# Optimization experiments

Hardware: AMD Instinct MI355X
Metric: run time of the kernel (lower is better)

Reference implementation:

```python
import jax, jax.numpy as jnp
import numpy as np

EPS = 1e-5

def conv1d(x, w, stride=2):
    # x: [N, Cin, L], w: [Cout, Cin, K], VALID padding
    return jax.lax.conv_general_dilated(x, w, (stride,), 'VALID',
                                         dimension_numbers=('NCH', 'OIH', 'NCH'))

def ln(x, g, b):
    # LayerNorm over last dim
    mu = jnp.mean(x, axis=-1, keepdims=True)
    var = jnp.mean((x - mu) ** 2, axis=-1, keepdims=True)
    return (x - mu) * jax.lax.rsqrt(var + EPS) * g + b

def block(x, w, g, b):
    return jax.nn.relu(ln(conv1d(x, w), g, b))

def setup_inputs() -> dict:
    key = jax.random.key(0)
    ks = jax.random.split(key, 20)
    B, CH, H, W = 4096, 143, 8, 8
    def p(k, shape, fan_in):
        return jax.random.normal(k, shape, dtype=jnp.float32) * (1.0 / np.sqrt(fan_in))
    inp = {
        'x': jax.random.normal(ks[0], (B, CH, H, W), dtype=jnp.float32),
        'w1': p(ks[1], (16, 2, 3), 6),
        'w2': p(ks[2], (28, 16, 3), 48),
        'w3': p(ks[3], (28, 28, 3), 84),
        'w4': p(ks[4], (28, 28, 3), 84),
        'f1': p(ks[5], (4, 2, 3), 6),
        'f2': p(ks[6], (4, 4, 3), 12),
        'f3': p(ks[7], (4, 4, 3), 12),
        'f4': p(ks[8], (4, 4, 3), 12),
        'ln1_w': jnp.ones((71,), jnp.float32), 'ln1_b': jnp.zeros((71,), jnp.float32),
        'ln2_w': jnp.ones((35,), jnp.float32), 'ln2_b': jnp.zeros((35,), jnp.float32),
        'ln3_w': jnp.ones((17,), jnp.float32), 'ln3_b': jnp.zeros((17,), jnp.float32),
        'ln4_w': jnp.ones((8,), jnp.float32), 'ln4_b': jnp.zeros((8,), jnp.float32),
    }
    return inp

def reference(x, w1, w2, w3, w4, f1, f2, f3, f4,
              ln1_w, ln1_b, ln2_w, ln2_b, ln3_w, ln3_b, ln4_w, ln4_b):
    b, ch, h, w = x.shape
    cr = x[:, :, 3:5, :]   # [b, ch, 2, w]
    cc = x[:, :, :, 3:5]   # [b, ch, h, 2]
    # FFT magnitude along spectral axis (axis=1)
    cr_fft = jnp.abs(jnp.fft.fft(cr, axis=1)).astype(jnp.float32)
    cc_fft = jnp.abs(jnp.fft.fft(cc, axis=1)).astype(jnp.float32)
    # reshape to [b*w (or b*h), 2, ch] sequences
    cr = jnp.transpose(cr, (0, 2, 3, 1)).reshape(b * w, 2, ch)
    cc = jnp.transpose(cc, (0, 2, 3, 1)).reshape(b * h, 2, ch)
    cr_fft = jnp.transpose(cr_fft, (0, 2, 3, 1)).reshape(b * w, 2, ch)
    cc_fft = jnp.transpose(cc_fft, (0, 2, 3, 1)).reshape(b * h, 2, ch)
    # spatial towers: 143 -> 71 -> 35 -> 17 -> 8, channels 2->16->28->28->28
    cr = block(cr, w1, ln1_w, ln1_b); cc = block(cc, w1, ln1_w, ln1_b)
    cr = block(cr, w2, ln2_w, ln2_b); cc = block(cc, w2, ln2_w, ln2_b)
    cr = block(cr, w3, ln3_w, ln3_b); cc = block(cc, w3, ln3_w, ln3_b)
    cr = block(cr, w4, ln4_w, ln4_b); cc = block(cc, w4, ln4_w, ln4_b)
    # fft towers: channels 2->4->4->4->4
    cr_fft = block(cr_fft, f1, ln1_w, ln1_b); cc_fft = block(cc_fft, f1, ln1_w, ln1_b)
    cr_fft = block(cr_fft, f2, ln2_w, ln2_b); cc_fft = block(cc_fft, f2, ln2_w, ln2_b)
    cr_fft = block(cr_fft, f3, ln3_w, ln3_b); cc_fft = block(cc_fft, f3, ln3_w, ln3_b)
    cr_fft = block(cr_fft, f4, ln4_w, ln4_b); cc_fft = block(cc_fft, f4, ln4_w, ln4_b)
    cr = jnp.transpose(cr.reshape(b, w, -1, 8), (0, 2, 1, 3))          # [b,28,w,8]
    cc = jnp.transpose(cc.reshape(b, h, -1, 8), (0, 2, 1, 3))          # [b,28,h,8]
    cr_fft = jnp.transpose(cr_fft.reshape(b, w, -1, 8), (0, 2, 1, 3))  # [b,4,w,8]
    cc_fft = jnp.transpose(cc_fft.reshape(b, h, -1, 8), (0, 2, 1, 3))  # [b,4,h,8]
    return jnp.concatenate([cr, cc, cr_fft, cc_fft], axis=1)           # [b,64,8,8]
```

## Files before the change

kernel.cpp:

```cpp
#include <hip/hip_runtime.h>
#include <math.h>

typedef _Float16 h16;
typedef _Float16 h16x2 __attribute__((ext_vector_type(2)));

#define NS 65536
#define VSTR 131072

__global__ __launch_bounds__(256) void k_gather(const float* __restrict__ x,
                                                float* __restrict__ xv,
                                                float* __restrict__ tw) {
  const int b = blockIdx.x;
  if (b < 4096) {
    const float* xb = x + (size_t)b * 9152;
    const int base = b * 32;
    for (int i = threadIdx.x; i < 9152; i += 256) {
      float v = xb[i];
      int c = i >> 6, pos = i & 63;
      if (pos >= 24 && pos < 40)
        xv[(size_t)c * VSTR + base + (pos - 24)] = v;
      int wc = pos & 7;
      if (wc == 3 || wc == 4)
        xv[(size_t)c * VSTR + base + 16 + ((pos >> 3) << 1) + (wc - 3)] = v;
    }
  } else {
    for (int i = threadIdx.x; i < 10296; i += 256) {
      int k = i / 143, n = i - k * 143;
      int e = (k * n) % 143;
      float ang = 6.2831853071795864769f * (float)e / 143.0f;
      float s, c;
      sincosf(ang, &s, &c);
      tw[2 * i] = c;
      tw[2 * i + 1] = s;
    }
  }
}

__global__ __launch_bounds__(256, 2) void k_dft(const float* __restrict__ xv,
                                                const float* __restrict__ tw,
                                                h16* __restrict__ fm) {
  const int v = blockIdx.x * 256 + threadIdx.x;
  float xr[143];
#pragma unroll
  for (int n = 0; n < 143; ++n) xr[n] = xv[(size_t)n * VSTR + v];

  for (int k = 0; k < 72; ++k) {
    const float* __restrict__ twk = tw + k * 286;
    float re = 0.f, im = 0.f;
#pragma unroll
    for (int n = 0; n < 143; ++n) {
      re = fmaf(xr[n], twk[2 * n], re);
      im = fmaf(xr[n], twk[2 * n + 1], im);
    }
    float m = sqrtf(re * re + im * im);
    fm[(size_t)k * VSTR + v] = (h16)m;
    if (k) fm[(size_t)(143 - k) * VSTR + v] = (h16)m;
  }
}

__device__ __forceinline__ void smap(int& d, int& w, int& va, int& vb,
                                     int& bi, int& u) {
  int lane = threadIdx.x & 63;
  w = __builtin_amdgcn_readfirstlane(threadIdx.x >> 6);
  d = (int)blockIdx.x * 64 + lane;
  bi = d >> 4;
  u = d & 15;
  va = (u < 8) ? bi * 32 + ((u >> 2) << 3) + ((u & 3) << 1)
               : bi * 32 + 16 + ((u & 7) << 1);
  vb = va + 1;
}

__global__ __launch_bounds__(256, 2) void k_c1(const float* __restrict__ xv,
                                               const h16* __restrict__ fm,
                                               const float* __restrict__ w1,
                                               const float* __restrict__ f1,
                                               float* __restrict__ s1) {
  int d, w, va, vb, bi, u;
  smap(d, w, va, vb, bi, u);

  {
    float sum[4] = {0, 0, 0, 0}, sq[4] = {0, 0, 0, 0};
    float A0 = xv[va], B0 = xv[vb];
    for (int p = 0; p < 71; ++p) {
      float A1 = xv[(size_t)(2 * p + 1) * VSTR + va];
      float A2 = xv[(size_t)(2 * p + 2) * VSTR + va];
      float B1 = xv[(size_t)(2 * p + 1) * VSTR + vb];
      float B2 = xv[(size_t)(2 * p + 2) * VSTR + vb];
#pragma unroll
      for (int j = 0; j < 4; ++j) {
        const float* wp = w1 + (4 * w + j) * 6;
        float v = A0 * wp[0];
        v = fmaf(A1, wp[1], v); v = fmaf(A2, wp[2], v);
        v = fmaf(B0, wp[3], v); v = fmaf(B1, wp[4], v); v = fmaf(B2, wp[5], v);
        sum[j] += v; sq[j] = fmaf(v, v, sq[j]);
      }
      A0 = A2; B0 = B2;
    }
#pragma unroll
    for (int j = 0; j < 4; ++j) {
      float mu = sum[j] * (1.0f / 71.0f);
      float var = sq[j] * (1.0f / 71.0f) - mu * mu;
      s1[(size_t)(4 * w + j) * NS + d] = mu;
      s1[(size_t)(16 + 4 * w + j) * NS + d] = rsqrtf(var + 1e-5f);
    }
  }
  {
    float sum = 0.f, sq = 0.f;
    const float* wp = f1 + w * 6;
    float A0 = (float)fm[va], B0 = (float)fm[vb];
    for (int p = 0; p < 71; ++p) {
      float A1 = (float)fm[(size_t)(2 * p + 1) * VSTR + va];
      float A2 = (float)fm[(size_t)(2 * p + 2) * VSTR + va];
      float B1 = (float)fm[(size_t)(2 * p + 1) * VSTR + vb];
      float B2 = (float)fm[(size_t)(2 * p + 2) * VSTR + vb];
      float v = A0 * wp[0];
      v = fmaf(A1, wp[1], v); v = fmaf(A2, wp[2], v);
      v = fmaf(B0, wp[3], v); v = fmaf(B1, wp[4], v); v = fmaf(B2, wp[5], v);
      sum += v; sq = fmaf(v, v, sq);
      A0 = A2; B0 = B2;
    }
    float mu = sum * (1.0f / 71.0f);
    float var = sq * (1.0f / 71.0f) - mu * mu;
    s1[(size_t)(32 + w) * NS + d] = mu;
    s1[(size_t)(36 + w) * NS + d] = rsqrtf(var + 1e-5f);
  }
}

__global__ __launch_bounds__(256, 2) void k_c2(const float* __restrict__ xv,
                                               const h16* __restrict__ fm,
                                               const float* __restrict__ w1,
                                               const float* __restrict__ w2,
                                               const float* __restrict__ f1,
                                               const float* __restrict__ f2,
                                               const float* __restrict__ l1g,
                                               const float* __restrict__ l1b,
                                               const float* __restrict__ s1,
                                               h16* __restrict__ z2,
                                               float* __restrict__ s2) {
  __shared__ float red[4][32][64];
  const int lane = threadIdx.x & 63;
  const int w = threadIdx.x >> 6;
  const int d = (int)blockIdx.x * 64 + lane;
  const int bi = d >> 4, u = d & 15;
  const int va = (u < 8) ? bi * 32 + ((u >> 2) << 3) + ((u & 3) << 1)
                         : bi * 32 + 16 + ((u & 7) << 1);
  const int ps = w * 9;
  const int pe = (ps + 9 < 35) ? (ps + 9) : 35;

  float sum[28], sq[28];
  float sums[4], sqs[4];

  {
    float mu1[16], inv1[16];
#pragma unroll
    for (int c = 0; c < 16; ++c) {
      mu1[c] = s1[(size_t)c * NS + d];
      inv1[c] = s1[(size_t)(16 + c) * NS + d];
    }
#pragma unroll
    for (int j = 0; j < 28; ++j) { sum[j] = 0.f; sq[j] = 0.f; }

    float n0[16], n1[16], n2[16];
    float a2, b2, a3, b3, a4, b4, a5, b5, a6, b6;

    {
      float2 r0 = *(const float2*)(xv + (size_t)(4 * ps) * VSTR + va);
      float2 r1 = *(const float2*)(xv + (size_t)(4 * ps + 1) * VSTR + va);
      float2 r2 = *(const float2*)(xv + (size_t)(4 * ps + 2) * VSTR + va);
      a2 = r2.x; b2 = r2.y;
      const float gg = l1g[2 * ps], bb = l1b[2 * ps];
#pragma unroll
      for (int c = 0; c < 16; ++c) {
        const float* wp = w1 + c * 6;
        float v = r0.x * wp[0];
        v = fmaf(r1.x, wp[1], v); v = fmaf(a2, wp[2], v);
        v = fmaf(r0.y, wp[3], v); v = fmaf(r1.y, wp[4], v); v = fmaf(b2, wp[5], v);
        n0[c] = fmaxf(fmaf((v - mu1[c]) * inv1[c], gg, bb), 0.f);
      }
      float2 r3 = *(const float2*)(xv + (size_t)(4 * ps + 3) * VSTR + va);
      float2 r4 = *(const float2*)(xv + (size_t)(4 * ps + 4) * VSTR + va);
      float2 r5 = *(const float2*)(xv + (size_t)(4 * ps + 5) * VSTR + va);
      float2 r6 = *(const float2*)(xv + (size_t)(4 * ps + 6) * VSTR + va);
      a3 = r3.x; b3 = r3.y; a4 = r4.x; b4 = r4.y;
      a5 = r5.x; b5 = r5.y; a6 = r6.x; b6 = r6.y;
    }

#pragma unroll 1
    for (int p = ps; p < pe; ++p) {
      {
        const float gg = l1g[2 * p + 1], bb = l1b[2 * p + 1];
#pragma unroll
        for (int c = 0; c < 16; ++c) {
          const float* wp = w1 + c * 6;
          float v = a2 * wp[0];
          v = fmaf(a3, wp[1], v); v = fmaf(a4, wp[2], v);
          v = fmaf(b2, wp[3], v); v = fmaf(b3, wp[4], v); v = fmaf(b4, wp[5], v);
          n1[c] = fmaxf(fmaf((v - mu1[c]) * inv1[c], gg, bb), 0.f);
        }
      }
      {
        const float gg = l1g[2 * p + 2], bb = l1b[2 * p + 2];
#pragma unroll
        for (int c = 0; c < 16; ++c) {
          const float* wp = w1 + c * 6;
          float v = a4 * wp[0];
          v = fmaf(a5, wp[1], v); v = fmaf(a6, wp[2], v);
          v = fmaf(b4, wp[3], v); v = fmaf(b5, wp[4], v); v = fmaf(b6, wp[5], v);
          n2[c] = fmaxf(fmaf((v - mu1[c]) * inv1[c], gg, bb), 0.f);
        }
      }
      a2 = a6; b2 = b6;
      {
        const int rbase = (p < 34) ? (4 * p + 7) : 139;
        const float* rp = xv + (size_t)rbase * VSTR + va;
        float2 r3 = *(const float2*)(rp);
        float2 r4 = *(const float2*)(rp + (size_t)VSTR);
        float2 r5 = *(const float2*)(rp + (size_t)2 * VSTR);
        float2 r6 = *(const float2*)(rp + (size_t)3 * VSTR);
        a3 = r3.x; b3 = r3.y; a4 = r4.x; b4 = r4.y;
        a5 = r5.x; b5 = r5.y; a6 = r6.x; b6 = r6.y;
      }
#pragma unroll
      for (int j = 0; j < 28; ++j) {
        const float* wp = w2 + j * 48;
        float acc = 0.f;
#pragma unroll
        for (int ci = 0; ci < 16; ++ci) {
          acc = fmaf(n0[ci], wp[ci * 3 + 0], acc);
          acc = fmaf(n1[ci], wp[ci * 3 + 1], acc);
          acc = fmaf(n2[ci], wp[ci * 3 + 2], acc);
        }
        z2[(size_t)(j * 35 + p) * NS + d] = (h16)acc;
        sum[j] += acc; sq[j] = fmaf(acc, acc, sq[j]);
      }
#pragma unroll
      for (int c = 0; c < 16; ++c) n0[c] = n2[c];
    }
  }

  {
    float mu1[4], inv1[4];
#pragma unroll
    for (int c = 0; c < 4; ++c) {
      mu1[c] = s1[(size_t)(32 + c) * NS + d];
      inv1[c] = s1[(size_t)(36 + c) * NS + d];
    }
#pragma unroll
    for (int c = 0; c < 4; ++c) { sums[c] = 0.f; sqs[c] = 0.f; }
    float n0[4], n1[4], n2[4];
    float a2, b2, a3, b3, a4, b4, a5, b5, a6, b6;

    {
      h16x2 r0 = *(const h16x2*)(fm + (size_t)(4 * ps) * VSTR + va);
      h16x2 r1 = *(const h16x2*)(fm + (size_t)(4 * ps + 1) * VSTR + va);
      h16x2 r2 = *(const h16x2*)(fm + (size_t)(4 * ps + 2) * VSTR + va);
      float a0 = (float)r0.x, b0 = (float)r0.y;
      float a1 = (float)r1.x, b1 = (float)r1.y;
      a2 = (float)r2.x; b2 = (float)r2.y;
      const float gg = l1g[2 * ps], bb = l1b[2 * ps];
#pragma unroll
      for (int c = 0; c < 4; ++c) {
        const float* wp = f1 + c * 6;
        float v = a0 * wp[0];
        v = fmaf(a1, wp[1], v); v = fmaf(a2, wp[2], v);
        v = fmaf(b0, wp[3], v); v = fmaf(b1, wp[4], v); v = fmaf(b2, wp[5], v);
        n0[c] = fmaxf(fmaf((v - mu1[c]) * inv1[c], gg, bb), 0.f);
      }
      h16x2 r3 = *(const h16x2*)(fm + (size_t)(4 * ps + 3) * VSTR + va);
      h16x2 r4 = *(const h16x2*)(fm + (size_t)(4 * ps + 4) * VSTR + va);
      h16x2 r5 = *(const h16x2*)(fm + (size_t)(4 * ps + 5) * VSTR + va);
      h16x2 r6 = *(const h16x2*)(fm + (size_t)(4 * ps + 6) * VSTR + va);
      a3 = (float)r3.x; b3 = (float)r3.y; a4 = (float)r4.x; b4 = (float)r4.y;
      a5 = (float)r5.x; b5 = (float)r5.y; a6 = (float)r6.x; b6 = (float)r6.y;
    }

#pragma unroll 1
    for (int p = ps; p < pe; ++p) {
      {
        const float gg = l1g[2 * p + 1], bb = l1b[2 * p + 1];
#pragma unroll
        for (int c = 0; c < 4; ++c) {
          const float* wp = f1 + c * 6;
          float v = a2 * wp[0];
          v = fmaf(a3, wp[1], v); v = fmaf(a4, wp[2], v);
          v = fmaf(b2, wp[3], v); v = fmaf(b3, wp[4], v); v = fmaf(b4, wp[5], v);
          n1[c] = fmaxf(fmaf((v - mu1[c]) * inv1[c], gg, bb), 0.f);
        }
      }
      {
        const float gg = l1g[2 * p + 2], bb = l1b[2 * p + 2];
#pragma unroll
        for (int c = 0; c < 4; ++c) {
          const float* wp = f1 + c * 6;
          float v = a4 * wp[0];
          v = fmaf(a5, wp[1], v); v = fmaf(a6, wp[2], v);
          v = fmaf(b4, wp[3], v); v = fmaf(b5, wp[4], v); v = fmaf(b6, wp[5], v);
          n2[c] = fmaxf(fmaf((v - mu1[c]) * inv1[c], gg, bb), 0.f);
        }
      }
      a2 = a6; b2 = b6;
      {
        const int rbase = (p < 34) ? (4 * p + 7) : 139;
        const h16* rp = fm + (size_t)rbase * VSTR + va;
        h16x2 r3 = *(const h16x2*)(rp);
        h16x2 r4 = *(const h16x2*)(rp + (size_t)VSTR);
        h16x2 r5 = *(const h16x2*)(rp + (size_t)2 * VSTR);
        h16x2 r6 = *(const h16x2*)(rp + (size_t)3 * VSTR);
        a3 = (float)r3.x; b3 = (float)r3.y; a4 = (float)r4.x; b4 = (float)r4.y;
        a5 = (float)r5.x; b5 = (float)r5.y; a6 = (float)r6.x; b6 = (float)r6.y;
      }
#pragma unroll
      for (int co = 0; co < 4; ++co) {
        const float* wpo = f2 + co * 12;
        float acc = 0.f;
#pragma unroll
        for (int c = 0; c < 4; ++c) acc = fmaf(n0[c], wpo[c * 3 + 0], acc);
#pragma unroll
        for (int c = 0; c < 4; ++c) acc = fmaf(n1[c], wpo[c * 3 + 1], acc);
#pragma unroll
        for (int c = 0; c < 4; ++c) acc = fmaf(n2[c], wpo[c * 3 + 2], acc);
        z2[(size_t)(980 + co * 35 + p) * NS + d] = (h16)acc;
        sums[co] += acc; sqs[co] = fmaf(acc, acc, sqs[co]);
      }
#pragma unroll
      for (int c = 0; c < 4; ++c) n0[c] = n2[c];
    }
  }

#pragma unroll
  for (int j = 0; j < 28; ++j) red[w][j][lane] = sum[j];
#pragma unroll
  for (int c = 0; c < 4; ++c) red[w][28 + c][lane] = sums[c];
  __syncthreads();
  const int jb = 7 * w;
  float fs[7], fq[7];
#pragma unroll
  for (int t = 0; t < 7; ++t)
    fs[t] = red[0][jb + t][lane] + red[1][jb + t][lane] +
            red[2][jb + t][lane] + red[3][jb + t][lane];
  float fss = red[0][28 + w][lane] + red[1][28 + w][lane] +
              red[2][28 + w][lane] + red[3][28 + w][lane];
  __syncthreads();
#pragma unroll
  for (int j = 0; j < 28; ++j) red[w][j][lane] = sq[j];
#pragma unroll
  for (int c = 0; c < 4; ++c) red[w][28 + c][lane] = sqs[c];
  __syncthreads();
#pragma unroll
  for (int t = 0; t < 7; ++t)
    fq[t] = red[0][jb + t][lane] + red[1][jb + t][lane] +
            red[2][jb + t][lane] + red[3][jb + t][lane];
  float fqs = red[0][28 + w][lane] + red[1][28 + w][lane] +
              red[2][28 + w][lane] + red[3][28 + w][lane];
#pragma unroll
  for (int t = 0; t < 7; ++t) {
    float mu = fs[t] * (1.0f / 35.0f);
    float var = fq[t] * (1.0f / 35.0f) - mu * mu;
    s2[(size_t)(jb + t) * NS + d] = mu;
    s2[(size_t)(28 + jb + t) * NS + d] = rsqrtf(var + 1e-5f);
  }
  {
    float mu = fss * (1.0f / 35.0f);
    float var = fqs * (1.0f / 35.0f) - mu * mu;
    s2[(size_t)(56 + w) * NS + d] = mu;
    s2[(size_t)(60 + w) * NS + d] = rsqrtf(var + 1e-5f);
  }
}

__global__ __launch_bounds__(256, 1) void k_c3(const h16* __restrict__ z2,
                                               const float* __restrict__ w3,
                                               const float* __restrict__ f3,
                                               const float* __restrict__ l2g,
                                               const float* __restrict__ l2b,
                                               const float* __restrict__ s2,
                                               h16* __restrict__ z3,
                                               float* __restrict__ s3) {
  int d, w, va, vb, bi, u;
  smap(d, w, va, vb, bi, u);

  {
    float acc[7][17];
#pragma unroll
    for (int j = 0; j < 7; ++j)
#pragma unroll
      for (int p = 0; p < 17; ++p) acc[j][p] = 0.f;
    const int cobase = 7 * w;
#pragma unroll 1
    for (int ci = 0; ci < 28; ++ci) {
      float mu = s2[(size_t)ci * NS + d];
      float inv = s2[(size_t)(28 + ci) * NS + d];
      float n[35];
#pragma unroll
      for (int t = 0; t < 35; ++t) {
        float raw = (float)z2[(size_t)(ci * 35 + t) * NS + d];
        n[t] = fmaxf(fmaf((raw - mu) * inv, l2g[t], l2b[t]), 0.f);
      }
#pragma unroll
      for (int j = 0; j < 7; ++j) {
        const float* wp = w3 + (cobase + j) * 84 + ci * 3;
        float w0 = wp[0], w1v = wp[1], w2v = wp[2];
#pragma unroll
        for (int p = 0; p < 17; ++p)
          acc[j][p] = fmaf(n[2 * p], w0,
                      fmaf(n[2 * p + 1], w1v,
                      fmaf(n[2 * p + 2], w2v, acc[j][p])));
      }
    }
#pragma unroll
    for (int j = 0; j < 7; ++j) {
      const int co = cobase + j;
      float sum = 0.f, sq = 0.f;
#pragma unroll
      for (int p = 0; p < 17; ++p) {
        sum += acc[j][p]; sq = fmaf(acc[j][p], acc[j][p], sq);
        z3[(size_t)(co * 17 + p) * NS + d] = (h16)acc[j][p];
      }
      float mu = sum * (1.0f / 17.0f);
      float var = sq * (1.0f / 17.0f) - mu * mu;
      s3[(size_t)co * NS + d] = mu;
      s3[(size_t)(28 + co) * NS + d] = rsqrtf(var + 1e-5f);
    }
  }
  {
    float acc[17];
#pragma unroll
    for (int p = 0; p < 17; ++p) acc[p] = 0.f;
    const int co = w;
#pragma unroll 1
    for (int ci = 0; ci < 4; ++ci) {
      float mu = s2[(size_t)(56 + ci) * NS + d];
      float inv = s2[(size_t)(60 + ci) * NS + d];
      float n[35];
#pragma unroll
      for (int t = 0; t < 35; ++t) {
        float raw = (float)z2[(size_t)(980 + ci * 35 + t) * NS + d];
        n[t] = fmaxf(fmaf((raw - mu) * inv, l2g[t], l2b[t]), 0.f);
      }
      const float* wp = f3 + co * 12 + ci * 3;
      float w0 = wp[0], w1v = wp[1], w2v = wp[2];
#pragma unroll
      for (int p = 0; p < 17; ++p)
        acc[p] = fmaf(n[2 * p], w0,
                 fmaf(n[2 * p + 1], w1v,
                 fmaf(n[2 * p + 2], w2v, acc[p])));
    }
    float sum = 0.f, sq = 0.f;
#pragma unroll
    for (int p = 0; p < 17; ++p) {
      sum += acc[p]; sq = fmaf(acc[p], acc[p], sq);
      z3[(size_t)(476 + co * 17 + p) * NS + d] = (h16)acc[p];
    }
    float mu = sum * (1.0f / 17.0f);
    float var = sq * (1.0f / 17.0f) - mu * mu;
    s3[(size_t)(56 + co) * NS + d] = mu;
    s3[(size_t)(60 + co) * NS + d] = rsqrtf(var + 1e-5f);
  }
}

__global__ __launch_bounds__(256, 1) void k_c4(const h16* __restrict__ z3,
                                               const float* __restrict__ w4,
                                               const float* __restrict__ f4,
                                               const float* __restrict__ l3g,
                                               const float* __restrict__ l3b,
                                               const float* __restrict__ l4g,
                                               const float* __restrict__ l4b,
                                               const float* __restrict__ s3,
                                               float* __restrict__ out) {
  int d, w, va, vb, bi, u;
  smap(d, w, va, vb, bi, u);

  {
    float acc[7][8];
#pragma unroll
    for (int j = 0; j < 7; ++j)
#pragma unroll
      for (int p = 0; p < 8; ++p) acc[j][p] = 0.f;
    const int cobase = 7 * w;
#pragma unroll 1
    for (int ci = 0; ci < 28; ++ci) {
      float mu = s3[(size_t)ci * NS + d];
      float inv = s3[(size_t)(28 + ci) * NS + d];
      float n[17];
#pragma unroll
      for (int t = 0; t < 17; ++t) {
        float raw = (float)z3[(size_t)(ci * 17 + t) * NS + d];
        n[t] = fmaxf(fmaf((raw - mu) * inv, l3g[t], l3b[t]), 0.f);
      }
#pragma unroll
      for (int j = 0; j < 7; ++j) {
        const float* wp = w4 + (cobase + j) * 84 + ci * 3;
        float w0 = wp[0], w1v = wp[1], w2v = wp[2];
#pragma unroll
        for (int p = 0; p < 8; ++p)
          acc[j][p] = fmaf(n[2 * p], w0,
                      fmaf(n[2 * p + 1], w1v,
                      fmaf(n[2 * p + 2], w2v, acc[j][p])));
      }
    }
#pragma unroll
    for (int j = 0; j < 7; ++j) {
      const int co = cobase + j;
      float sum = 0.f, sq = 0.f;
#pragma unroll
      for (int p = 0; p < 8; ++p) { sum += acc[j][p]; sq = fmaf(acc[j][p], acc[j][p], sq); }
      float mu = sum * 0.125f;
      float var = sq * 0.125f - mu * mu;
      float inv = rsqrtf(var + 1e-5f);
      const int ch = (u < 8) ? co : (28 + co);
      float* op = out + (size_t)bi * 4096 + (size_t)ch * 64 + (size_t)(u & 7) * 8;
      float o[8];
#pragma unroll
      for (int p = 0; p < 8; ++p)
        o[p] = fmaxf(fmaf((acc[j][p] - mu) * inv, l4g[p], l4b[p]), 0.f);
      *(float4*)(op) = make_float4(o[0], o[1], o[2], o[3]);
      *(float4*)(op + 4) = make_float4(o[4], o[5], o[6], o[7]);
    }
  }
  {
    float acc[8];
#pragma unroll
    for (int p = 0; p < 8; ++p) acc[p] = 0.f;
    const int co = w;
#pragma unroll 1
    for (int ci = 0; ci < 4; ++ci) {
      float mu = s3[(size_t)(56 + ci) * NS + d];
      float inv = s3[(size_t)(60 + ci) * NS + d];
      float n[17];
#pragma unroll
      for (int t = 0; t < 17; ++t) {
        float raw = (float)z3[(size_t)(476 + ci * 17 + t) * NS + d];
        n[t] = fmaxf(fmaf((raw - mu) * inv, l3g[t], l3b[t]), 0.f);
      }
      const float* wp = f4 + co * 12 + ci * 3;
      float w0 = wp[0], w1v = wp[1], w2v = wp[2];
#pragma unroll
      for (int p = 0; p < 8; ++p)
        acc[p] = fmaf(n[2 * p], w0,
                 fmaf(n[2 * p + 1], w1v,
                 fmaf(n[2 * p + 2], w2v, acc[p])));
    }
    float sum = 0.f, sq = 0.f;
#pragma unroll
    for (int p = 0; p < 8; ++p) { sum += acc[p]; sq = fmaf(acc[p], acc[p], sq); }
    float mu = sum * 0.125f;
    float var = sq * 0.125f - mu * mu;
    float inv = rsqrtf(var + 1e-5f);
    const int ch = (u < 8) ? (56 + co) : (60 + co);
    float* op = out + (size_t)bi * 4096 + (size_t)ch * 64 + (size_t)(u & 7) * 8;
    float o[8];
#pragma unroll
    for (int p = 0; p < 8; ++p)
      o[p] = fmaxf(fmaf((acc[p] - mu) * inv, l4g[p], l4b[p]), 0.f);
    *(float4*)(op) = make_float4(o[0], o[1], o[2], o[3]);
    *(float4*)(op + 4) = make_float4(o[4], o[5], o[6], o[7]);
  }
}

extern "C" void kernel_launch(void* const* d_in, const int* in_sizes, int n_in,
                              void* d_out, int out_size, void* d_ws, size_t ws_size,
                              hipStream_t stream) {
  const float* x   = (const float*)d_in[0];
  const float* w1  = (const float*)d_in[1];
  const float* w2  = (const float*)d_in[2];
  const float* w3  = (const float*)d_in[3];
  const float* w4  = (const float*)d_in[4];
  const float* f1  = (const float*)d_in[5];
  const float* f2  = (const float*)d_in[6];
  const float* f3  = (const float*)d_in[7];
  const float* f4  = (const float*)d_in[8];
  const float* l1g = (const float*)d_in[9];
  const float* l1b = (const float*)d_in[10];
  const float* l2g = (const float*)d_in[11];
  const float* l2b = (const float*)d_in[12];
  const float* l3g = (const float*)d_in[13];
  const float* l3b = (const float*)d_in[14];
  const float* l4g = (const float*)d_in[15];
  const float* l4b = (const float*)d_in[16];
  float* out = (float*)d_out;
  char* wsb = (char*)d_ws;

  float* xv = (float*)(wsb + 0);
  h16*   fm = (h16*)(wsb + 74973184ull);
  h16*   z2 = (h16*)(wsb + 112459776ull);
  h16*   z3 = (h16*)(wsb + 259260416ull);
  float* s1 = (float*)(wsb + 330563584ull);
  float* s2 = (float*)(wsb + 341049344ull);
  float* s3 = (float*)(wsb + 357826560ull);
  float* tw = (float*)(wsb + 374603776ull);

  k_gather<<<4097, 256, 0, stream>>>(x, xv, tw);
  k_dft<<<512, 256, 0, stream>>>(xv, tw, fm);
  k_c1<<<1024, 256, 0, stream>>>(xv, fm, w1, f1, s1);
  k_c2<<<1024, 256, 0, stream>>>(xv, fm, w1, w2, f1, f2, l1g, l1b, s1, z2, s2);
  k_c3<<<1024, 256, 0, stream>>>(z2, w3, f3, l2g, l2b, s2, z3, s3);
  k_c4<<<1024, 256, 0, stream>>>(z3, w4, f4, l3g, l3b, l4g, l4b, s3, out);
}
```

Before: 1.161 ms.

## Fuse conv3 and conv4 stages into one kernel via shared-memory staging

Merges the third and fourth conv+LayerNorm stages into a single kernel. Normalized layer-3 activations are staged in LDS as fp16 instead of writing z3 and its statistics to global memory and reading them back. This removes a kernel launch and a large global round trip. In exchange the kernel takes more LDS, adds block barriers, and raises launch bounds to two blocks per CU, which may pressure registers given the large accumulator arrays.

```diff
diff --git a/kernel.cpp b/kernel.cpp
--- a/kernel.cpp
+++ b/kernel.cpp
@@ -367,16 +367,25 @@
   }
 }
 
-__global__ __launch_bounds__(256, 1) void k_c3(const h16* __restrict__ z2,
-                                               const float* __restrict__ w3,
-                                               const float* __restrict__ f3,
-                                               const float* __restrict__ l2g,
-                                               const float* __restrict__ l2b,
-                                               const float* __restrict__ s2,
-                                               h16* __restrict__ z3,
-                                               float* __restrict__ s3) {
-  int d, w, va, vb, bi, u;
-  smap(d, w, va, vb, bi, u);
+__global__ __launch_bounds__(256, 2) void k_c34(const h16* __restrict__ z2,
+                                                const float* __restrict__ w3,
+                                                const float* __restrict__ w4,
+                                                const float* __restrict__ f3,
+                                                const float* __restrict__ f4,
+                                                const float* __restrict__ l2g,
+                                                const float* __restrict__ l2b,
+                                                const float* __restrict__ l3g,
+                                                const float* __restrict__ l3b,
+                                                const float* __restrict__ l4g,
+                                                const float* __restrict__ l4b,
+                                                const float* __restrict__ s2,
+                                                float* __restrict__ out) {
+  __shared__ h16 nb[28][17][64];
+  const int lane = threadIdx.x & 63;
+  const int w = threadIdx.x >> 6;
+  const int d = (int)blockIdx.x * 64 + lane;
+  const int bi = d >> 4, u = d & 15;
+  const int cobase = 7 * w;
 
   {
     float acc[7][17];
@@ -384,7 +393,6 @@
     for (int j = 0; j < 7; ++j)
 #pragma unroll
       for (int p = 0; p < 17; ++p) acc[j][p] = 0.f;
-    const int cobase = 7 * w;
 #pragma unroll 1
     for (int ci = 0; ci < 28; ++ci) {
       float mu = s2[(size_t)ci * NS + d];
@@ -408,19 +416,63 @@
     }
 #pragma unroll
     for (int j = 0; j < 7; ++j) {
+      float sum = 0.f, sq = 0.f;
+#pragma unroll
+      for (int p = 0; p < 17; ++p) { sum += acc[j][p]; sq = fmaf(acc[j][p], acc[j][p], sq); }
+      float mu = sum * (1.0f / 17.0f);
+      float var = sq * (1.0f / 17.0f) - mu * mu;
+      float inv = rsqrtf(var + 1e-5f);
+#pragma unroll
+      for (int p = 0; p < 17; ++p)
+        nb[cobase + j][p][lane] =
+            (h16)fmaxf(fmaf((acc[j][p] - mu) * inv, l3g[p], l3b[p]), 0.f);
+    }
+  }
+  __syncthreads();
+
+  {
+    float a4[7][8];
+#pragma unroll
+    for (int j = 0; j < 7; ++j)
+#pragma unroll
+      for (int p = 0; p < 8; ++p) a4[j][p] = 0.f;
+#pragma unroll 1
+    for (int ci = 0; ci < 28; ++ci) {
+      float n[17];
+#pragma unroll
+      for (int t = 0; t < 17; ++t) n[t] = (float)nb[ci][t][lane];
+#pragma unroll
+      for (int j = 0; j < 7; ++j) {
+        const float* wp = w4 + (cobase + j) * 84 + ci * 3;
+        float w0 = wp[0], w1v = wp[1], w2v = wp[2];
+#pragma unroll
+        for (int p = 0; p < 8; ++p)
+          a4[j][p] = fmaf(n[2 * p], w0,
+                     fmaf(n[2 * p + 1], w1v,
+                     fmaf(n[2 * p + 2], w2v, a4[j][p])));
+      }
+    }
+#pragma unroll
+    for (int j = 0; j < 7; ++j) {
       const int co = cobase + j;
       float sum = 0.f, sq = 0.f;
 #pragma unroll
-      for (int p = 0; p < 17; ++p) {
-        sum += acc[j][p]; sq = fmaf(acc[j][p], acc[j][p], sq);
-        z3[(size_t)(co * 17 + p) * NS + d] = (h16)acc[j][p];
-      }
-      float mu = sum * (1.0f / 17.0f);
-      float var = sq * (1.0f / 17.0f) - mu * mu;
-      s3[(size_t)co * NS + d] = mu;
-      s3[(size_t)(28 + co) * NS + d] = rsqrtf(var + 1e-5f);
-    }
-  }
+      for (int p = 0; p < 8; ++p) { sum += a4[j][p]; sq = fmaf(a4[j][p], a4[j][p], sq); }
+      float mu = sum * 0.125f;
+      float var = sq * 0.125f - mu * mu;
+      float inv = rsqrtf(var + 1e-5f);
+      const int ch = (u < 8) ? co : (28 + co);
+      float* op = out + (size_t)bi * 4096 + (size_t)ch * 64 + (size_t)(u & 7) * 8;
+      float o[8];
+#pragma unroll
+      for (int p = 0; p < 8; ++p)
+        o[p] = fmaxf(fmaf((a4[j][p] - mu) * inv, l4g[p], l4b[p]), 0.f);
+      *(float4*)(op) = make_float4(o[0], o[1], o[2], o[3]);
+      *(float4*)(op + 4) = make_float4(o[4], o[5], o[6], o[7]);
+    }
+  }
+  __syncthreads();
+
   {
     float acc[17];
 #pragma unroll
@@ -446,102 +498,38 @@
     }
     float sum = 0.f, sq = 0.f;
 #pragma unroll
-    for (int p = 0; p < 17; ++p) {
-      sum += acc[p]; sq = fmaf(acc[p], acc[p], sq);
-      z3[(size_t)(476 + co * 17 + p) * NS + d] = (h16)acc[p];
-    }
+    for (int p = 0; p < 17; ++p) { sum += acc[p]; sq = fmaf(acc[p], acc[p], sq); }
     float mu = sum * (1.0f / 17.0f);
     float var = sq * (1.0f / 17.0f) - mu * mu;
-    s3[(size_t)(56 + co) * NS + d] = mu;
-    s3[(size_t)(60 + co) * NS + d] = rsqrtf(var + 1e-5f);
-  }
-}
-
-__global__ __launch_bounds__(256, 1) void k_c4(const h16* __restrict__ z3,
-                                               const float* __restrict__ w4,
-                                               const float* __restrict__ f4,
-                                               const float* __restrict__ l3g,
-                                               const float* __restrict__ l3b,
-                                               const float* __restrict__ l4g,
-                                               const float* __restrict__ l4b,
-                                               const float* __restrict__ s3,
-                                               float* __restrict__ out) {
-  int d, w, va, vb, bi, u;
-  smap(d, w, va, vb, bi, u);
-
-  {
-    float acc[7][8];
-#pragma unroll
-    for (int j = 0; j < 7; ++j)
-#pragma unroll
-      for (int p = 0; p < 8; ++p) acc[j][p] = 0.f;
-    const int cobase = 7 * w;
-#pragma unroll 1
-    for (int ci = 0; ci < 28; ++ci) {
-      float mu = s3[(size_t)ci * NS + d];
-      float inv = s3[(size_t)(28 + ci) * NS + d];
-      float n[17];
-#pragma unroll
-      for (int t = 0; t < 17; ++t) {
-        float raw = (float)z3[(size_t)(ci * 17 + t) * NS + d];
-        n[t] = fmaxf(fmaf((raw - mu) * inv, l3g[t], l3b[t]), 0.f);
-      }
-#pragma unroll
-      for (int j = 0; j < 7; ++j) {
-        const float* wp = w4 + (cobase + j) * 84 + ci * 3;
-        float w0 = wp[0], w1v = wp[1], w2v = wp[2];
-#pragma unroll
-        for (int p = 0; p < 8; ++p)
-          acc[j][p] = fmaf(n[2 * p], w0,
-                      fmaf(n[2 * p + 1], w1v,
-                      fmaf(n[2 * p + 2], w2v, acc[j][p])));
-      }
-    }
-#pragma unroll
-    for (int j = 0; j < 7; ++j) {
-      const int co = cobase + j;
-      float sum = 0.f, sq = 0.f;
-#pragma unroll
-      for (int p = 0; p < 8; ++p) { sum += acc[j][p]; sq = fmaf(acc[j][p], acc[j][p], sq); }
-      float mu = sum * 0.125f;
-      float var = sq * 0.125f - mu * mu;
-      float inv = rsqrtf(var + 1e-5f);
-      const int ch = (u < 8) ? co : (28 + co);
-      float* op = out + (size_t)bi * 4096 + (size_t)ch * 64 + (size_t)(u & 7) * 8;
-      float o[8];
-#pragma unroll
-      for (int p = 0; p < 8; ++p)
-        o[p] = fmaxf(fmaf((acc[j][p] - mu) * inv, l4g[p], l4b[p]), 0.f);
-      *(float4*)(op) = make_float4(o[0], o[1], o[2], o[3]);
-      *(float4*)(op + 4) = make_float4(o[4], o[5], o[6], o[7]);
-    }
-  }
-  {
-    float acc[8];
-#pragma unroll
-    for (int p = 0; p < 8; ++p) acc[p] = 0.f;
+    float inv = rsqrtf(var + 1e-5f);
+#pragma unroll
+    for (int p = 0; p < 17; ++p)
+      nb[w][p][lane] =
+          (h16)fmaxf(fmaf((acc[p] - mu) * inv, l3g[p], l3b[p]), 0.f);
+  }
+  __syncthreads();
+
+  {
+    float a4[8];
+#pragma unroll
+    for (int p = 0; p < 8; ++p) a4[p] = 0.f;
     const int co = w;
 #pragma unroll 1
     for (int ci = 0; ci < 4; ++ci) {
-      float mu = s3[(size_t)(56 + ci) * NS + d];
-      float inv = s3[(size_t)(60 + ci) * NS + d];
       float n[17];
 #pragma unroll
-      for (int t = 0; t < 17; ++t) {
-        float raw = (float)z3[(size_t)(476 + ci * 17 + t) * NS + d];
-        n[t] = fmaxf(fmaf((raw - mu) * inv, l3g[t], l3b[t]), 0.f);
-      }
+      for (int t = 0; t < 17; ++t) n[t] = (float)nb[ci][t][lane];
       const float* wp = f4 + co * 12 + ci * 3;
       float w0 = wp[0], w1v = wp[1], w2v = wp[2];
 #pragma unroll
       for (int p = 0; p < 8; ++p)
-        acc[p] = fmaf(n[2 * p], w0,
-                 fmaf(n[2 * p + 1], w1v,
-                 fmaf(n[2 * p + 2], w2v, acc[p])));
+        a4[p] = fmaf(n[2 * p], w0,
+                fmaf(n[2 * p + 1], w1v,
+                fmaf(n[2 * p + 2], w2v, a4[p])));
     }
     float sum = 0.f, sq = 0.f;
 #pragma unroll
-    for (int p = 0; p < 8; ++p) { sum += acc[p]; sq = fmaf(acc[p], acc[p], sq); }
+    for (int p = 0; p < 8; ++p) { sum += a4[p]; sq = fmaf(a4[p], a4[p], sq); }
     float mu = sum * 0.125f;
     float var = sq * 0.125f - mu * mu;
     float inv = rsqrtf(var + 1e-5f);
@@ -550,7 +538,7 @@
     float o[8];
 #pragma unroll
     for (int p = 0; p < 8; ++p)
-      o[p] = fmaxf(fmaf((acc[p] - mu) * inv, l4g[p], l4b[p]), 0.f);
+      o[p] = fmaxf(fmaf((a4[p] - mu) * inv, l4g[p], l4b[p]), 0.f);
     *(float4*)(op) = make_float4(o[0], o[1], o[2], o[3]);
     *(float4*)(op + 4) = make_float4(o[4], o[5], o[6], o[7]);
   }
@@ -582,16 +570,14 @@
   float* xv = (float*)(wsb + 0);
   h16*   fm = (h16*)(wsb + 74973184ull);
   h16*   z2 = (h16*)(wsb + 112459776ull);
-  h16*   z3 = (h16*)(wsb + 259260416ull);
   float* s1 = (float*)(wsb + 330563584ull);
   float* s2 = (float*)(wsb + 341049344ull);
-  float* s3 = (float*)(wsb + 357826560ull);
   float* tw = (float*)(wsb + 374603776ull);
 
   k_gather<<<4097, 256, 0, stream>>>(x, xv, tw);
   k_dft<<<512, 256, 0, stream>>>(xv, tw, fm);
   k_c1<<<1024, 256, 0, stream>>>(xv, fm, w1, f1, s1);
   k_c2<<<1024, 256, 0, stream>>>(xv, fm, w1, w2, f1, f2, l1g, l1b, s1, z2, s2);
-  k_c3<<<1024, 256, 0, stream>>>(z2, w3, f3, l2g, l2b, s2, z3, s3);
-  k_c4<<<1024, 256, 0, stream>>>(z3, w4, f4, l3g, l3b, l4g, l4b, s3, out);
-}
+  k_c34<<<1024, 256, 0, stream>>>(z2, w3, w4, f3, f4, l2g, l2b, l3g, l3b, l4g, l4b,
+                                  s2, out);
+}
```

Measured after the change: 1.872 ms. +61.2%, slower.

## Fuse layer-1 stats kernel into layer-2 kernel with block-level LDS reduction

Applied to the files above, without the earlier changes.

Merges k_c1 into k_c2. Layer-1 LayerNorm mean and inverse-std are now computed inside the same block by splitting the 71 output positions across the four waves and reducing the partial sums through shared memory. This removes one kernel launch and the global round trip of the s1 statistics buffer. In exchange the reduction work is repartitioned, extra barriers are added, and register pressure in the fused kernel rises (20 partial sums plus sq), which may hurt occupancy.

```diff
diff --git a/kernel.cpp b/kernel.cpp
--- a/kernel.cpp
+++ b/kernel.cpp
@@ -70,73 +70,16 @@
   vb = va + 1;
 }
 
-__global__ __launch_bounds__(256, 2) void k_c1(const float* __restrict__ xv,
-                                               const h16* __restrict__ fm,
-                                               const float* __restrict__ w1,
-                                               const float* __restrict__ f1,
-                                               float* __restrict__ s1) {
-  int d, w, va, vb, bi, u;
-  smap(d, w, va, vb, bi, u);
-
-  {
-    float sum[4] = {0, 0, 0, 0}, sq[4] = {0, 0, 0, 0};
-    float A0 = xv[va], B0 = xv[vb];
-    for (int p = 0; p < 71; ++p) {
-      float A1 = xv[(size_t)(2 * p + 1) * VSTR + va];
-      float A2 = xv[(size_t)(2 * p + 2) * VSTR + va];
-      float B1 = xv[(size_t)(2 * p + 1) * VSTR + vb];
-      float B2 = xv[(size_t)(2 * p + 2) * VSTR + vb];
-#pragma unroll
-      for (int j = 0; j < 4; ++j) {
-        const float* wp = w1 + (4 * w + j) * 6;
-        float v = A0 * wp[0];
-        v = fmaf(A1, wp[1], v); v = fmaf(A2, wp[2], v);
-        v = fmaf(B0, wp[3], v); v = fmaf(B1, wp[4], v); v = fmaf(B2, wp[5], v);
-        sum[j] += v; sq[j] = fmaf(v, v, sq[j]);
-      }
-      A0 = A2; B0 = B2;
-    }
-#pragma unroll
-    for (int j = 0; j < 4; ++j) {
-      float mu = sum[j] * (1.0f / 71.0f);
-      float var = sq[j] * (1.0f / 71.0f) - mu * mu;
-      s1[(size_t)(4 * w + j) * NS + d] = mu;
-      s1[(size_t)(16 + 4 * w + j) * NS + d] = rsqrtf(var + 1e-5f);
-    }
-  }
-  {
-    float sum = 0.f, sq = 0.f;
-    const float* wp = f1 + w * 6;
-    float A0 = (float)fm[va], B0 = (float)fm[vb];
-    for (int p = 0; p < 71; ++p) {
-      float A1 = (float)fm[(size_t)(2 * p + 1) * VSTR + va];
-      float A2 = (float)fm[(size_t)(2 * p + 2) * VSTR + va];
-      float B1 = (float)fm[(size_t)(2 * p + 1) * VSTR + vb];
-      float B2 = (float)fm[(size_t)(2 * p + 2) * VSTR + vb];
-      float v = A0 * wp[0];
-      v = fmaf(A1, wp[1], v); v = fmaf(A2, wp[2], v);
-      v = fmaf(B0, wp[3], v); v = fmaf(B1, wp[4], v); v = fmaf(B2, wp[5], v);
-      sum += v; sq = fmaf(v, v, sq);
-      A0 = A2; B0 = B2;
-    }
-    float mu = sum * (1.0f / 71.0f);
-    float var = sq * (1.0f / 71.0f) - mu * mu;
-    s1[(size_t)(32 + w) * NS + d] = mu;
-    s1[(size_t)(36 + w) * NS + d] = rsqrtf(var + 1e-5f);
-  }
-}
-
-__global__ __launch_bounds__(256, 2) void k_c2(const float* __restrict__ xv,
-                                               const h16* __restrict__ fm,
-                                               const float* __restrict__ w1,
-                                               const float* __restrict__ w2,
-                                               const float* __restrict__ f1,
-                                               const float* __restrict__ f2,
-                                               const float* __restrict__ l1g,
-                                               const float* __restrict__ l1b,
-                                               const float* __restrict__ s1,
-                                               h16* __restrict__ z2,
-                                               float* __restrict__ s2) {
+__global__ __launch_bounds__(256, 2) void k_c12(const float* __restrict__ xv,
+                                                const h16* __restrict__ fm,
+                                                const float* __restrict__ w1,
+                                                const float* __restrict__ w2,
+                                                const float* __restrict__ f1,
+                                                const float* __restrict__ f2,
+                                                const float* __restrict__ l1g,
+                                                const float* __restrict__ l1b,
+                                                h16* __restrict__ z2,
+                                                float* __restrict__ s2) {
   __shared__ float red[4][32][64];
   const int lane = threadIdx.x & 63;
   const int w = threadIdx.x >> 6;
@@ -144,8 +87,77 @@
   const int bi = d >> 4, u = d & 15;
   const int va = (u < 8) ? bi * 32 + ((u >> 2) << 3) + ((u & 3) << 1)
                          : bi * 32 + 16 + ((u & 7) << 1);
-  const int ps = w * 9;
-  const int pe = (ps + 9 < 35) ? (ps + 9) : 35;
+
+  {
+    float ps[20], pq[20];
+#pragma unroll
+    for (int j = 0; j < 20; ++j) { ps[j] = 0.f; pq[j] = 0.f; }
+    const int ips = 18 * w;
+    const int ipe = (ips + 18 < 71) ? (ips + 18) : 71;
+    float2 r0 = *(const float2*)(xv + (size_t)(2 * ips) * VSTR + va);
+    float A0 = r0.x, B0 = r0.y;
+    h16x2 g0 = *(const h16x2*)(fm + (size_t)(2 * ips) * VSTR + va);
+    float FA0 = (float)g0.x, FB0 = (float)g0.y;
+#pragma unroll 1
+    for (int ip = ips; ip < ipe; ++ip) {
+      float2 r1 = *(const float2*)(xv + (size_t)(2 * ip + 1) * VSTR + va);
+      float2 r2 = *(const float2*)(xv + (size_t)(2 * ip + 2) * VSTR + va);
+      h16x2 g1 = *(const h16x2*)(fm + (size_t)(2 * ip + 1) * VSTR + va);
+      h16x2 g2 = *(const h16x2*)(fm + (size_t)(2 * ip + 2) * VSTR + va);
+#pragma unroll
+      for (int c = 0; c < 16; ++c) {
+        const float* wp = w1 + c * 6;
+        float v = A0 * wp[0];
+        v = fmaf(r1.x, wp[1], v); v = fmaf(r2.x, wp[2], v);
+        v = fmaf(B0, wp[3], v); v = fmaf(r1.y, wp[4], v); v = fmaf(r2.y, wp[5], v);
+        ps[c] += v; pq[c] = fmaf(v, v, pq[c]);
+      }
+      float FA1 = (float)g1.x, FB1 = (float)g1.y;
+      float FA2 = (float)g2.x, FB2 = (float)g2.y;
+#pragma unroll
+      for (int c = 0; c < 4; ++c) {
+        const float* wp = f1 + c * 6;
+        float v = FA0 * wp[0];
+        v = fmaf(FA1, wp[1], v); v = fmaf(FA2, wp[2], v);
+        v = fmaf(FB0, wp[3], v); v = fmaf(FB1, wp[4], v); v = fmaf(FB2, wp[5], v);
+        ps[16 + c] += v; pq[16 + c] = fmaf(v, v, pq[16 + c]);
+      }
+      A0 = r2.x; B0 = r2.y; FA0 = FA2; FB0 = FB2;
+    }
+#pragma unroll
+    for (int j = 0; j < 20; ++j) red[w][j][lane] = ps[j];
+    __syncthreads();
+    float ts[5];
+#pragma unroll
+    for (int t = 0; t < 5; ++t) {
+      int c = 5 * w + t;
+      ts[t] = red[0][c][lane] + red[1][c][lane] + red[2][c][lane] + red[3][c][lane];
+    }
+    __syncthreads();
+#pragma unroll
+    for (int j = 0; j < 20; ++j) red[w][j][lane] = pq[j];
+    __syncthreads();
+    float tmu[5], tiv[5];
+#pragma unroll
+    for (int t = 0; t < 5; ++t) {
+      int c = 5 * w + t;
+      float tq = red[0][c][lane] + red[1][c][lane] + red[2][c][lane] + red[3][c][lane];
+      float mu = ts[t] * (1.0f / 71.0f);
+      float var = tq * (1.0f / 71.0f) - mu * mu;
+      tmu[t] = mu; tiv[t] = rsqrtf(var + 1e-5f);
+    }
+    __syncthreads();
+#pragma unroll
+    for (int t = 0; t < 5; ++t) {
+      int c = 5 * w + t;
+      red[0][c][lane] = tmu[t];
+      red[1][c][lane] = tiv[t];
+    }
+    __syncthreads();
+  }
+
+  const int ps2 = w * 9;
+  const int pe2 = (ps2 + 9 < 35) ? (ps2 + 9) : 35;
 
   float sum[28], sq[28];
   float sums[4], sqs[4];
@@ -154,8 +166,8 @@
     float mu1[16], inv1[16];
 #pragma unroll
     for (int c = 0; c < 16; ++c) {
-      mu1[c] = s1[(size_t)c * NS + d];
-      inv1[c] = s1[(size_t)(16 + c) * NS + d];
+      mu1[c] = red[0][c][lane];
+      inv1[c] = red[1][c][lane];
     }
 #pragma unroll
     for (int j = 0; j < 28; ++j) { sum[j] = 0.f; sq[j] = 0.f; }
@@ -164,11 +176,11 @@
     float a2, b2, a3, b3, a4, b4, a5, b5, a6, b6;
 
     {
-      float2 r0 = *(const float2*)(xv + (size_t)(4 * ps) * VSTR + va);
-      float2 r1 = *(const float2*)(xv + (size_t)(4 * ps + 1) * VSTR + va);
-      float2 r2 = *(const float2*)(xv + (size_t)(4 * ps + 2) * VSTR + va);
+      float2 r0 = *(const float2*)(xv + (size_t)(4 * ps2) * VSTR + va);
+      float2 r1 = *(const float2*)(xv + (size_t)(4 * ps2 + 1) * VSTR + va);
+      float2 r2 = *(const float2*)(xv + (size_t)(4 * ps2 + 2) * VSTR + va);
       a2 = r2.x; b2 = r2.y;
-      const float gg = l1g[2 * ps], bb = l1b[2 * ps];
+      const float gg = l1g[2 * ps2], bb = l1b[2 * ps2];
 #pragma unroll
       for (int c = 0; c < 16; ++c) {
         const float* wp = w1 + c * 6;
@@ -177,16 +189,16 @@
         v = fmaf(r0.y, wp[3], v); v = fmaf(r1.y, wp[4], v); v = fmaf(b2, wp[5], v);
         n0[c] = fmaxf(fmaf((v - mu1[c]) * inv1[c], gg, bb), 0.f);
       }
-      float2 r3 = *(const float2*)(xv + (size_t)(4 * ps + 3) * VSTR + va);
-      float2 r4 = *(const float2*)(xv + (size_t)(4 * ps + 4) * VSTR + va);
-      float2 r5 = *(const float2*)(xv + (size_t)(4 * ps + 5) * VSTR + va);
-      float2 r6 = *(const float2*)(xv + (size_t)(4 * ps + 6) * VSTR + va);
+      float2 r3 = *(const float2*)(xv + (size_t)(4 * ps2 + 3) * VSTR + va);
+      float2 r4 = *(const float2*)(xv + (size_t)(4 * ps2 + 4) * VSTR + va);
+      float2 r5 = *(const float2*)(xv + (size_t)(4 * ps2 + 5) * VSTR + va);
+      float2 r6 = *(const float2*)(xv + (size_t)(4 * ps2 + 6) * VSTR + va);
       a3 = r3.x; b3 = r3.y; a4 = r4.x; b4 = r4.y;
       a5 = r5.x; b5 = r5.y; a6 = r6.x; b6 = r6.y;
     }
 
 #pragma unroll 1
-    for (int p = ps; p < pe; ++p) {
+    for (int p = ps2; p < pe2; ++p) {
       {
         const float gg = l1g[2 * p + 1], bb = l1b[2 * p + 1];
 #pragma unroll
@@ -242,8 +254,8 @@
     float mu1[4], inv1[4];
 #pragma unroll
     for (int c = 0; c < 4; ++c) {
-      mu1[c] = s1[(size_t)(32 + c) * NS + d];
-      inv1[c] = s1[(size_t)(36 + c) * NS + d];
+      mu1[c] = red[0][16 + c][lane];
+      inv1[c] = red[1][16 + c][lane];
     }
 #pragma unroll
     for (int c = 0; c < 4; ++c) { sums[c] = 0.f; sqs[c] = 0.f; }
@@ -251,13 +263,13 @@
     float a2, b2, a3, b3, a4, b4, a5, b5, a6, b6;
 
     {
-      h16x2 r0 = *(const h16x2*)(fm + (size_t)(4 * ps) * VSTR + va);
-      h16x2 r1 = *(const h16x2*)(fm + (size_t)(4 * ps + 1) * VSTR + va);
-      h16x2 r2 = *(const h16x2*)(fm + (size_t)(4 * ps + 2) * VSTR + va);
+      h16x2 r0 = *(const h16x2*)(fm + (size_t)(4 * ps2) * VSTR + va);
+      h16x2 r1 = *(const h16x2*)(fm + (size_t)(4 * ps2 + 1) * VSTR + va);
+      h16x2 r2 = *(const h16x2*)(fm + (size_t)(4 * ps2 + 2) * VSTR + va);
       float a0 = (float)r0.x, b0 = (float)r0.y;
       float a1 = (float)r1.x, b1 = (float)r1.y;
       a2 = (float)r2.x; b2 = (float)r2.y;
-      const float gg = l1g[2 * ps], bb = l1b[2 * ps];
+      const float gg = l1g[2 * ps2], bb = l1b[2 * ps2];
 #pragma unroll
       for (int c = 0; c < 4; ++c) {
         const float* wp = f1 + c * 6;
@@ -266,16 +278,16 @@
         v = fmaf(b0, wp[3], v); v = fmaf(b1, wp[4], v); v = fmaf(b2, wp[5], v);
         n0[c] = fmaxf(fmaf((v - mu1[c]) * inv1[c], gg, bb), 0.f);
       }
-      h16x2 r3 = *(const h16x2*)(fm + (size_t)(4 * ps + 3) * VSTR + va);
-      h16x2 r4 = *(const h16x2*)(fm + (size_t)(4 * ps + 4) * VSTR + va);
-      h16x2 r5 = *(const h16x2*)(fm + (size_t)(4 * ps + 5) * VSTR + va);
-      h16x2 r6 = *(const h16x2*)(fm + (size_t)(4 * ps + 6) * VSTR + va);
+      h16x2 r3 = *(const h16x2*)(fm + (size_t)(4 * ps2 + 3) * VSTR + va);
+      h16x2 r4 = *(const h16x2*)(fm + (size_t)(4 * ps2 + 4) * VSTR + va);
+      h16x2 r5 = *(const h16x2*)(fm + (size_t)(4 * ps2 + 5) * VSTR + va);
+      h16x2 r6 = *(const h16x2*)(fm + (size_t)(4 * ps2 + 6) * VSTR + va);
       a3 = (float)r3.x; b3 = (float)r3.y; a4 = (float)r4.x; b4 = (float)r4.y;
       a5 = (float)r5.x; b5 = (float)r5.y; a6 = (float)r6.x; b6 = (float)r6.y;
     }
 
 #pragma unroll 1
-    for (int p = ps; p < pe; ++p) {
+    for (int p = ps2; p < pe2; ++p) {
       {
         const float gg = l1g[2 * p + 1], bb = l1b[2 * p + 1];
 #pragma unroll
@@ -327,6 +339,7 @@
     }
   }
 
+  __syncthreads();
 #pragma unroll
   for (int j = 0; j < 28; ++j) red[w][j][lane] = sum[j];
 #pragma unroll
@@ -583,15 +596,13 @@
   h16*   fm = (h16*)(wsb + 74973184ull);
   h16*   z2 = (h16*)(wsb + 112459776ull);
   h16*   z3 = (h16*)(wsb + 259260416ull);
-  float* s1 = (float*)(wsb + 330563584ull);
   float* s2 = (float*)(wsb + 341049344ull);
   float* s3 = (float*)(wsb + 357826560ull);
   float* tw = (float*)(wsb + 374603776ull);
 
   k_gather<<<4097, 256, 0, stream>>>(x, xv, tw);
   k_dft<<<512, 256, 0, stream>>>(xv, tw, fm);
-  k_c1<<<1024, 256, 0, stream>>>(xv, fm, w1, f1, s1);
-  k_c2<<<1024, 256, 0, stream>>>(xv, fm, w1, w2, f1, f2, l1g, l1b, s1, z2, s2);
+  k_c12<<<1024, 256, 0, stream>>>(xv, fm, w1, w2, f1, f2, l1g, l1b, z2, s2);
   k_c3<<<1024, 256, 0, stream>>>(z2, w3, f3, l2g, l2b, s2, z3, s3);
   k_c4<<<1024, 256, 0, stream>>>(z3, w4, f4, l3g, l3b, l4g, l4b, s3, out);
 }
```

Measured after the change: 1.147 ms. About the same (-1.2%).
